# Kernel optimization log

Measured on AMD Instinct MI355X. Metric: run time of the kernel, lower is better.

## Reference

```python
import jax, jax.numpy as jnp
import numpy as np
import math

B, S, D, H = 2, 2048, 1024, 16
DK = D // H


def setup_inputs() -> dict:
    key = jax.random.key(0)
    ks = jax.random.split(key, 12)
    scale = 1.0 / math.sqrt(D)
    inp = {
        "q": jax.random.normal(ks[0], (B, S, D), jnp.float32),
        "k": jax.random.normal(ks[1], (B, S, D), jnp.float32),
        "v": jax.random.normal(ks[2], (B, S, D), jnp.float32),
        # causal mask, broadcast over batch and heads; 0 entries are masked out
        "mask": jnp.tril(jnp.ones((S, S), jnp.int32))[None, None, :, :],
        "wq_w": jax.random.normal(ks[3], (D, D), jnp.float32) * scale,
        "wq_b": jax.random.normal(ks[4], (D,), jnp.float32) * 0.01,
        "wk_w": jax.random.normal(ks[5], (D, D), jnp.float32) * scale,
        "wk_b": jax.random.normal(ks[6], (D,), jnp.float32) * 0.01,
        "wv_w": jax.random.normal(ks[7], (D, D), jnp.float32) * scale,
        "wv_b": jax.random.normal(ks[8], (D,), jnp.float32) * 0.01,
        "wo_w": jax.random.normal(ks[9], (D, D), jnp.float32) * scale,
        "wo_b": jax.random.normal(ks[10], (D,), jnp.float32) * 0.01,
    }
    return inp


def _mha(q, k, v, mask, wq_w, wq_b, wk_w, wk_b, wv_w, wv_b, wo_w, wo_b):
    # nn.Linear: x @ W^T + b
    def split_heads(x):  # [B,S,D] -> [B,H,S,DK]
        return x.reshape(B, S, H, DK).transpose(0, 2, 1, 3)

    Q = split_heads(q @ wq_w.T + wq_b)
    K = split_heads(k @ wk_w.T + wk_b)
    V = split_heads(v @ wv_w.T + wv_b)

    scores = jnp.einsum("bhqd,bhkd->bhqk", Q, K) / math.sqrt(DK)  # [B,H,S,S]
    scores = jnp.where(mask == 0, jnp.float32(-1e9), scores)
    # NOTE: source uses softmax(dim=1) == over the HEADS axis; replicated faithfully.
    attn = jax.nn.softmax(scores, axis=1)
    out = jnp.einsum("bhqk,bhkd->bhqd", attn, V)  # [B,H,S,DK]
    out = out.transpose(0, 2, 1, 3).reshape(B, S, D)
    return out @ wo_w.T + wo_b


def reference(q, k, v, mask, wq_w, wq_b, wk_w, wk_b, wv_w, wv_b, wo_w, wo_b):
    return _mha(q, k, v, mask, wq_w, wq_b, wk_w, wk_b, wv_w, wv_b, wo_w, wo_b)
```

## Files before the change

kernel.cpp:

```cpp
#include <hip/hip_runtime.h>
#include <stdint.h>


#define BB 2
#define SS 2048
#define DD 1024
#define HH 16
#define DKK 64

typedef _Float16 f16;
typedef __attribute__((ext_vector_type(2))) _Float16 f16x2;
typedef __attribute__((ext_vector_type(8))) _Float16 f16x8;
typedef __attribute__((ext_vector_type(2))) __fp16 fp16x2_raw;
typedef __attribute__((ext_vector_type(4))) float f32x4;

typedef __attribute__((address_space(3))) uint32_t lds32_t;
typedef __attribute__((address_space(1))) uint32_t g32_t;

__device__ __forceinline__ void async_cp16(void* lds, const void* g){
    __builtin_amdgcn_global_load_lds((const g32_t*)g, (lds32_t*)lds, 16, 0, 0);
}

union U32H { uint32_t u; f16x2 h; fp16x2_raw hr; };

__device__ __forceinline__ uint32_t pk2(float a, float b){
    U32H c; c.hr = __builtin_amdgcn_cvt_pkrtz(a, b); return c.u;
}
__device__ __forceinline__ float h_lo(uint32_t w){ U32H c; c.u = w; return (float)c.h[0]; }
__device__ __forceinline__ float h_hi(uint32_t w){ U32H c; c.u = w; return (float)c.h[1]; }
__device__ __forceinline__ uint32_t pkmul(uint32_t a, uint32_t b){
    U32H x, y, r; x.u = a; y.u = b; r.h = x.h * y.h; return r.u;
}
__device__ __forceinline__ uint32_t pkadd(uint32_t a, uint32_t b){
    U32H x, y, r; x.u = a; y.u = b; r.h = x.h + y.h; return r.u;
}
__device__ __forceinline__ uint16_t f2h(float f){
    union { f16 h; uint16_t u; } c; c.h = (f16)f; return c.u;
}

__global__ __launch_bounds__(256) void cvt_all(
    const float* __restrict__ w0, const float* __restrict__ w1,
    const float* __restrict__ w2, const float* __restrict__ w3,
    const float* __restrict__ a0, const float* __restrict__ a1,
    const float* __restrict__ a2,
    uint16_t* __restrict__ dw0, uint16_t* __restrict__ dw1,
    uint16_t* __restrict__ dw2, uint16_t* __restrict__ dw3,
    uint16_t* __restrict__ da0, uint16_t* __restrict__ da1,
    uint16_t* __restrict__ da2)
{
    const int id = blockIdx.x;
    const float* s; uint16_t* d; int i;
    if (id < 4096) {
        const int y = id >> 10;
        s = (y==0) ? w0 : (y==1) ? w1 : (y==2) ? w2 : w3;
        d = (y==0) ? dw0 : (y==1) ? dw1 : (y==2) ? dw2 : dw3;
        i = (id & 1023) * 256 + threadIdx.x;
    } else {
        const int id2 = id - 4096;
        const int y = id2 >> 12;
        s = (y==0) ? a0 : (y==1) ? a1 : a2;
        d = (y==0) ? da0 : (y==1) ? da1 : da2;
        i = (id2 & 4095) * 256 + threadIdx.x;
    }
    float4 v = ((const float4*)s)[i];
    ((uint2*)d)[i] = make_uint2(pk2(v.x, v.y), pk2(v.z, v.w));
}

template <int OMODE, int SUMA>
__device__ __forceinline__ void gemm_core(
    uint16_t (*As)[32], uint16_t (*Bs)[32],
    const uint16_t* __restrict__ A, const uint16_t* __restrict__ W,
    const float* __restrict__ bias, void* __restrict__ Cout,
    const int kbeg, const int kend)
{
    const int t    = threadIdx.x;
    const int bm   = blockIdx.x * 128;
    const int bn   = blockIdx.y * 128;
    const int lane = t & 63;
    const int w    = t >> 6;
    const int wm   = (w >> 1) * 64;
    const int wn   = (w & 1) * 64;
    const int lm   = lane & 15;
    const int quad = lane >> 4;

    f32x4 acc[4][4] = {};

    const int lr = lane >> 2;
    const int lc = (lane & 3) * 8;
    const size_t PS = (size_t)BB * SS * DD;

    for (int k0 = kbeg; k0 < kend; k0 += 32) {
#pragma unroll
        for (int i2 = 0; i2 < 2; ++i2) {
            const int i = w * 2 + i2;
            const size_t aoff = (size_t)(bm + 16*i + lr) * DD + k0 + lc;
            if (SUMA) {
                uint4 u0 = *(const uint4*)&A[aoff];
                uint4 u1 = *(const uint4*)&A[aoff + PS];
                uint4 u2 = *(const uint4*)&A[aoff + 2*PS];
                uint4 u3 = *(const uint4*)&A[aoff + 3*PS];
                uint4 sm;
                sm.x = pkadd(pkadd(u0.x, u1.x), pkadd(u2.x, u3.x));
                sm.y = pkadd(pkadd(u0.y, u1.y), pkadd(u2.y, u3.y));
                sm.z = pkadd(pkadd(u0.z, u1.z), pkadd(u2.z, u3.z));
                sm.w = pkadd(pkadd(u0.w, u1.w), pkadd(u2.w, u3.w));
                *(uint4*)&As[16*i + lr][lc] = sm;
            } else {
                async_cp16(&As[16*i][0], &A[aoff]);
            }
            async_cp16(&Bs[16*i][0], &W[(size_t)(bn + 16*i + lr) * DD + k0 + lc]);
        }
        __syncthreads();
        f16x8 a8[4], b8[4];
#pragma unroll
        for (int mt = 0; mt < 4; ++mt) a8[mt] = *(const f16x8*)&As[wm + 16*mt + lm][quad*8];
#pragma unroll
        for (int nt = 0; nt < 4; ++nt) b8[nt] = *(const f16x8*)&Bs[wn + 16*nt + lm][quad*8];
#pragma unroll
        for (int mt = 0; mt < 4; ++mt)
#pragma unroll
            for (int nt = 0; nt < 4; ++nt)
                acc[mt][nt] = __builtin_amdgcn_mfma_f32_16x16x32_f16(a8[mt], b8[nt], acc[mt][nt], 0, 0, 0);
        __syncthreads();
    }

#pragma unroll
    for (int nt = 0; nt < 4; ++nt) {
        const int ng = bn + wn + 16*nt + lm;
        const float bv = bias ? bias[ng] : 0.0f;
#pragma unroll
        for (int mt = 0; mt < 4; ++mt) {
            const int m0 = bm + wm + 16*mt + quad*4;
            if (OMODE == 1) {
                const int bb = m0 >> 11, s0 = m0 & (SS - 1);
                const int hh = ng >> 6,  dk = ng & 63;
                uint2 wv;
                wv.x = pk2(acc[mt][nt][0] + bv, acc[mt][nt][1] + bv);
                wv.y = pk2(acc[mt][nt][2] + bv, acc[mt][nt][3] + bv);
                *(uint2*)&((uint16_t*)Cout)[(((size_t)(bb*HH + hh))*DKK + dk)*SS + s0] = wv;
            } else {
#pragma unroll
                for (int r = 0; r < 4; ++r) {
                    const int m = m0 + r;
                    const float val = acc[mt][nt][r] + bv;
                    if (OMODE == 0) {
                        const int bb = m >> 11, s = m & (SS - 1);
                        const int hh = ng >> 6, dk = ng & 63;
                        ((uint16_t*)Cout)[(((size_t)(bb*HH + hh))*SS + s)*DKK + dk] = f2h(val);
                    } else {
                        ((float*)Cout)[(size_t)m * DD + ng] = val;
                    }
                }
            }
        }
    }
}

__global__ __launch_bounds__(256) void gemm_qkv(
    const uint16_t* __restrict__ xq, const uint16_t* __restrict__ wq,
    const float* __restrict__ bq, uint16_t* __restrict__ Qc,
    const uint16_t* __restrict__ xk, const uint16_t* __restrict__ wk,
    const float* __restrict__ bk, uint16_t* __restrict__ Kc,
    const uint16_t* __restrict__ xv, const uint16_t* __restrict__ wv,
    const float* __restrict__ bv, uint16_t* __restrict__ Vt)
{
    __shared__ __align__(16) uint16_t As[128][32];
    __shared__ __align__(16) uint16_t Bs[128][32];
    const int z = blockIdx.z;
    if (z == 0)      gemm_core<0,0>(As, Bs, xq, wq, bq, Qc, 0, DD);
    else if (z == 1) gemm_core<0,0>(As, Bs, xk, wk, bk, Kc, 0, DD);
    else             gemm_core<1,0>(As, Bs, xv, wv, bv, Vt, 0, DD);
}

__global__ __launch_bounds__(256) void gemm_o_split(
    const uint16_t* __restrict__ A, const uint16_t* __restrict__ W,
    const float* __restrict__ bias, float* __restrict__ P0, float* __restrict__ P1)
{
    __shared__ __align__(16) uint16_t As[128][32];
    __shared__ __align__(16) uint16_t Bs[128][32];
    const int z = blockIdx.z;
    if (z == 0) gemm_core<2,1>(As, Bs, A, W, bias,    (void*)P0, 0,   512);
    else        gemm_core<2,1>(As, Bs, A, W, nullptr, (void*)P1, 512, 1024);
}

__global__ __launch_bounds__(256) void addf4(
    const float* __restrict__ a, const float* __restrict__ b, float* __restrict__ o)
{
    const int i = blockIdx.x * 256 + threadIdx.x;
    float4 x = ((const float4*)a)[i];
    float4 y = ((const float4*)b)[i];
    ((float4*)o)[i] = make_float4(x.x+y.x, x.y+y.y, x.z+y.z, x.w+y.w);
}

__global__ __launch_bounds__(1024) void suf_kernel(
    const uint16_t* __restrict__ Vt, float* __restrict__ Suf)
{
    const int bh = blockIdx.x;
    const int t  = threadIdx.x;
    const int d = t & 63, seg = t >> 6;
    __shared__ float cs[64][65];
    const uint16_t* row = Vt + ((size_t)bh * DKK + d) * SS;
#pragma unroll
    for (int cl = 0; cl < 4; ++cl) {
        const int c = seg * 4 + cl;
        float sum = 0.f;
#pragma unroll
        for (int jj = 0; jj < 4; ++jj) {
            uint4 u = *(const uint4*)&row[c * 32 + jj * 8];
            sum += ((h_lo(u.x)+h_hi(u.x)) + (h_lo(u.y)+h_hi(u.y)))
                 + ((h_lo(u.z)+h_hi(u.z)) + (h_lo(u.w)+h_hi(u.w)));
        }
        cs[c][d] = sum;
    }
    __syncthreads();
    if (t < 64) {
        float run = 0.f;
        Suf[((size_t)bh * 65 + 64) * DKK + t] = 0.f;
        for (int c = 63; c >= 0; --c) {
            run += cs[c][t];
            Suf[((size_t)bh * 65 + c) * DKK + t] = run;
        }
    }
}

__global__ __launch_bounds__(1024) void attn_v9(
    const uint16_t* __restrict__ Qc, const uint16_t* __restrict__ Kc,
    const uint16_t* __restrict__ Vt, const float* __restrict__ Suf,
    uint16_t* __restrict__ AOp)
{
    __shared__ __align__(16) uint16_t E[3][16][32][40];
    __shared__ __align__(16) uint16_t Zr[2][32][40];

    const int x  = blockIdx.x;
    const int p  = x & 3;
    const int b  = (x >> 2) & 1;
    const int pr = x >> 3;
    const int tid  = threadIdx.x;
    const int h    = tid >> 6;
    const int lane = tid & 63;
    const int lm   = lane & 15;
    const int quad = lane >> 4;

    const uint16_t* Qh = Qc + ((size_t)(b*HH + h)) * SS * DKK;
    const uint16_t* Kh = Kc + ((size_t)(b*HH + h)) * SS * DKK;
    const uint16_t* Vh = Vt + ((size_t)(b*HH + h)) * DKK * SS;
    uint16_t* AOb = AOp + ((size_t)(p*BB + b)) * SS * DD;

    const int rq  = tid >> 4;
    const int rk2 = tid & 15;

#pragma unroll
    for (int tt = 0; tt < 2; ++tt) {
        const int tq = tt ? (63 - pr) : pr;
        const int q0 = tq * 32;
        const int nch = (tq >= p) ? ((tq - p) >> 2) + 1 : 0;

        f16x8 qf[2][2];
#pragma unroll
        for (int qt = 0; qt < 2; ++qt)
#pragma unroll
            for (int kd = 0; kd < 2; ++kd)
                qf[qt][kd] = *(const f16x8*)&Qh[(size_t)(q0 + 16*qt + lm)*DKK + kd*32 + quad*8];

        f32x4 oacc[2][4] = {};

        auto SCORES = [&](int c, int ebw) {
            const int k0 = c * 32;
            f32x4 sacc[2][2] = {};
#pragma unroll
            for (int kt = 0; kt < 2; ++kt) {
                f16x8 kf0 = *(const f16x8*)&Kh[(size_t)(k0 + 16*kt + lm)*DKK + quad*8];
                f16x8 kf1 = *(const f16x8*)&Kh[(size_t)(k0 + 16*kt + lm)*DKK + 32 + quad*8];
#pragma unroll
                for (int qt = 0; qt < 2; ++qt) {
                    sacc[kt][qt] = __builtin_amdgcn_mfma_f32_16x16x32_f16(kf0, qf[qt][0], sacc[kt][qt], 0, 0, 0);
                    sacc[kt][qt] = __builtin_amdgcn_mfma_f32_16x16x32_f16(kf1, qf[qt][1], sacc[kt][qt], 0, 0, 0);
                }
            }
#pragma unroll
            for (int kt = 0; kt < 2; ++kt)
#pragma unroll
                for (int qt = 0; qt < 2; ++qt) {
                    const int qg = q0 + 16*qt + lm;
                    float e[4];
#pragma unroll
                    for (int r = 0; r < 4; ++r) {
                        const int kg = k0 + 16*kt + quad*4 + r;
                        e[r] = (kg > qg) ? 1.0f : __expf(sacc[kt][qt][r] * 0.125f);
                    }
                    *(uint2*)&E[ebw][h][16*qt + lm][16*kt + quad*4] =
                        make_uint2(pk2(e[0], e[1]), pk2(e[2], e[3]));
                }
        };

        auto HEADSUM = [&](int ebr, int zbw) {
            float z0 = 0.f, z1 = 0.f;
#pragma unroll
            for (int i = 0; i < 16; ++i) {
                uint32_t wv2 = *(const uint32_t*)&E[ebr][i][rq][rk2*2];
                z0 += h_lo(wv2); z1 += h_hi(wv2);
            }
            *(uint32_t*)&Zr[zbw][rq][rk2*2] = pk2(__fdividef(1.f, z0), __fdividef(1.f, z1));
        };

        auto PV = [&](int c, int ebr, int zbr) {
            const int k0 = c * 32;
            f16x8 vf[4];
#pragma unroll
            for (int dt = 0; dt < 4; ++dt)
                vf[dt] = *(const f16x8*)&Vh[(size_t)(16*dt + lm)*SS + k0 + quad*8];
#pragma unroll
            for (int qt = 0; qt < 2; ++qt) {
                uint4 eu = *(const uint4*)&E[ebr][h][16*qt + lm][quad*8];
                uint4 zu = *(const uint4*)&Zr[zbr][16*qt + lm][quad*8];
                union { uint4 u; f16x8 v; } P;
                P.u.x = pkmul(eu.x, zu.x); P.u.y = pkmul(eu.y, zu.y);
                P.u.z = pkmul(eu.z, zu.z); P.u.w = pkmul(eu.w, zu.w);
#pragma unroll
                for (int dt = 0; dt < 4; ++dt)
                    oacc[qt][dt] = __builtin_amdgcn_mfma_f32_16x16x32_f16(P.v, vf[dt], oacc[qt][dt], 0, 0, 0);
            }
        };

        __syncthreads();

        if (nch > 0) {
            SCORES(p, 0);
            __syncthreads();
            int eb = 0;
            for (int n = 0; n < nch; ++n) {
                const int c  = p + 4*n;
                const int zb = n & 1;
                if (tid < 512) HEADSUM(eb, zb);
                if (n > 0)       PV(c - 4, (eb + 2) % 3, zb ^ 1);
                if (n + 1 < nch) SCORES(c + 4, (eb + 1) % 3);
                __syncthreads();
                eb = (eb + 1 == 3) ? 0 : eb + 1;
            }
            PV(p + 4*(nch - 1), (eb + 2) % 3, (nch - 1) & 1);
        }

        float corr[4] = {0.f, 0.f, 0.f, 0.f};
        if (p == 0) {
            const float* Sf = Suf + ((size_t)(b*HH + h) * 65 + (tq + 1)) * DKK;
#pragma unroll
            for (int dt = 0; dt < 4; ++dt) corr[dt] = 0.0625f * Sf[16*dt + lm];
        }
#pragma unroll
        for (int qt = 0; qt < 2; ++qt)
#pragma unroll
            for (int dt = 0; dt < 4; ++dt)
#pragma unroll
                for (int r = 0; r < 4; ++r) {
                    const int s = q0 + 16*qt + quad*4 + r;
                    AOb[(size_t)s * DD + h*DKK + 16*dt + lm] = f2h(oacc[qt][dt][r] + corr[dt]);
                }
    }
}

extern "C" void kernel_launch(void* const* d_in, const int* in_sizes, int n_in,
                              void* d_out, int out_size, void* d_ws, size_t ws_size,
                              hipStream_t stream)
{
    const float* q    = (const float*)d_in[0];
    const float* k    = (const float*)d_in[1];
    const float* v    = (const float*)d_in[2];
    const float* wq_w = (const float*)d_in[4];
    const float* wq_b = (const float*)d_in[5];
    const float* wk_w = (const float*)d_in[6];
    const float* wk_b = (const float*)d_in[7];
    const float* wv_w = (const float*)d_in[8];
    const float* wv_b = (const float*)d_in[9];
    const float* wo_w = (const float*)d_in[10];
    const float* wo_b = (const float*)d_in[11];
    float* out = (float*)d_out;

    uint16_t* wsu = (uint16_t*)d_ws;
    const size_t M1 = (size_t)1 << 20;
    uint16_t* wcq = wsu + 0 * M1;
    uint16_t* wck = wsu + 1 * M1;
    uint16_t* wcv = wsu + 2 * M1;
    uint16_t* wco = wsu + 3 * M1;
    uint16_t* Qc  = wsu + 4 * M1;
    uint16_t* Kc  = wsu + 8 * M1;
    uint16_t* Vt  = wsu + 12 * M1;
    uint16_t* AOp = wsu + 16 * M1;
    uint16_t* xq  = wsu + 16 * M1;
    uint16_t* xk  = wsu + 20 * M1;
    uint16_t* xv  = wsu + 24 * M1;
    float*    Suf = (float*)wcq;
    float*    P1  = (float*)(wsu + 4 * M1);

    cvt_all<<<16384, 256, 0, stream>>>(
        wq_w, wk_w, wv_w, wo_w, q, k, v,
        wcq, wck, wcv, wco, xq, xk, xv);

    gemm_qkv<<<dim3(32, 8, 3), 256, 0, stream>>>(
        xq, wcq, wq_b, Qc,
        xk, wck, wk_b, Kc,
        xv, wcv, wv_b, Vt);

    suf_kernel<<<32, 1024, 0, stream>>>(Vt, Suf);
    attn_v9<<<256, 1024, 0, stream>>>(Qc, Kc, Vt, Suf, AOp);

    gemm_o_split<<<dim3(32, 8, 2), 256, 0, stream>>>(AOp, wco, wo_b, out, P1);
    addf4<<<4096, 256, 0, stream>>>(out, P1, out);
}
```

Measured before the change: 291.2 us.

## Split attention into one query tile per block, drop software pipelining

The attention kernel now launches 512 blocks, each handling a single 32-row query tile, where before 256 blocks each processed a paired light and heavy tile. The triple-buffered E and double-buffered Zr pipeline (scores of the next chunk overlapped with headsum and PV of the current one) is replaced by a plain sequential loop with three barriers per chunk. This cuts LDS use and aims for better occupancy and load balance across the larger grid. In exchange it gives up overlap between phases and adds synchronisation stalls, and the per-block work becomes more uneven because causal tiles differ in length.

```diff
diff --git a/kernel.cpp b/kernel.cpp
--- a/kernel.cpp
+++ b/kernel.cpp
@@ -223,18 +223,19 @@
     }
 }
 
-__global__ __launch_bounds__(1024) void attn_v9(
+__global__ __launch_bounds__(1024) void attn_v15(
     const uint16_t* __restrict__ Qc, const uint16_t* __restrict__ Kc,
     const uint16_t* __restrict__ Vt, const float* __restrict__ Suf,
     uint16_t* __restrict__ AOp)
 {
-    __shared__ __align__(16) uint16_t E[3][16][32][40];
-    __shared__ __align__(16) uint16_t Zr[2][32][40];
+    __shared__ __align__(16) uint16_t E[16][32][40];
+    __shared__ __align__(16) uint16_t Zr[32][40];
 
     const int x  = blockIdx.x;
     const int p  = x & 3;
     const int b  = (x >> 2) & 1;
-    const int pr = x >> 3;
+    const int j  = x >> 3;
+    const int tq = (j < 32) ? j : 95 - j;
     const int tid  = threadIdx.x;
     const int h    = tid >> 6;
     const int lane = tid & 63;
@@ -249,70 +250,65 @@
     const int rq  = tid >> 4;
     const int rk2 = tid & 15;
 
-#pragma unroll
-    for (int tt = 0; tt < 2; ++tt) {
-        const int tq = tt ? (63 - pr) : pr;
-        const int q0 = tq * 32;
-        const int nch = (tq >= p) ? ((tq - p) >> 2) + 1 : 0;
-
-        f16x8 qf[2][2];
-#pragma unroll
-        for (int qt = 0; qt < 2; ++qt)
-#pragma unroll
-            for (int kd = 0; kd < 2; ++kd)
-                qf[qt][kd] = *(const f16x8*)&Qh[(size_t)(q0 + 16*qt + lm)*DKK + kd*32 + quad*8];
-
-        f32x4 oacc[2][4] = {};
-
-        auto SCORES = [&](int c, int ebw) {
-            const int k0 = c * 32;
-            f32x4 sacc[2][2] = {};
-#pragma unroll
-            for (int kt = 0; kt < 2; ++kt) {
-                f16x8 kf0 = *(const f16x8*)&Kh[(size_t)(k0 + 16*kt + lm)*DKK + quad*8];
-                f16x8 kf1 = *(const f16x8*)&Kh[(size_t)(k0 + 16*kt + lm)*DKK + 32 + quad*8];
-#pragma unroll
-                for (int qt = 0; qt < 2; ++qt) {
-                    sacc[kt][qt] = __builtin_amdgcn_mfma_f32_16x16x32_f16(kf0, qf[qt][0], sacc[kt][qt], 0, 0, 0);
-                    sacc[kt][qt] = __builtin_amdgcn_mfma_f32_16x16x32_f16(kf1, qf[qt][1], sacc[kt][qt], 0, 0, 0);
+    const int q0 = tq * 32;
+
+    f16x8 qf[2][2];
+#pragma unroll
+    for (int qt = 0; qt < 2; ++qt)
+#pragma unroll
+        for (int kd = 0; kd < 2; ++kd)
+            qf[qt][kd] = *(const f16x8*)&Qh[(size_t)(q0 + 16*qt + lm)*DKK + kd*32 + quad*8];
+
+    f32x4 oacc[2][4] = {};
+
+    for (int c = p; c <= tq; c += 4) {
+        const int k0 = c * 32;
+        f32x4 sacc[2][2] = {};
+#pragma unroll
+        for (int kt = 0; kt < 2; ++kt) {
+            f16x8 kf0 = *(const f16x8*)&Kh[(size_t)(k0 + 16*kt + lm)*DKK + quad*8];
+            f16x8 kf1 = *(const f16x8*)&Kh[(size_t)(k0 + 16*kt + lm)*DKK + 32 + quad*8];
+#pragma unroll
+            for (int qt = 0; qt < 2; ++qt) {
+                sacc[kt][qt] = __builtin_amdgcn_mfma_f32_16x16x32_f16(kf0, qf[qt][0], sacc[kt][qt], 0, 0, 0);
+                sacc[kt][qt] = __builtin_amdgcn_mfma_f32_16x16x32_f16(kf1, qf[qt][1], sacc[kt][qt], 0, 0, 0);
+            }
+        }
+        __syncthreads();
+#pragma unroll
+        for (int kt = 0; kt < 2; ++kt)
+#pragma unroll
+            for (int qt = 0; qt < 2; ++qt) {
+                const int qg = q0 + 16*qt + lm;
+                float e[4];
+#pragma unroll
+                for (int r = 0; r < 4; ++r) {
+                    const int kg = k0 + 16*kt + quad*4 + r;
+                    e[r] = (kg > qg) ? 1.0f : __expf(sacc[kt][qt][r] * 0.125f);
                 }
-            }
-#pragma unroll
-            for (int kt = 0; kt < 2; ++kt)
-#pragma unroll
-                for (int qt = 0; qt < 2; ++qt) {
-                    const int qg = q0 + 16*qt + lm;
-                    float e[4];
-#pragma unroll
-                    for (int r = 0; r < 4; ++r) {
-                        const int kg = k0 + 16*kt + quad*4 + r;
-                        e[r] = (kg > qg) ? 1.0f : __expf(sacc[kt][qt][r] * 0.125f);
-                    }
-                    *(uint2*)&E[ebw][h][16*qt + lm][16*kt + quad*4] =
-                        make_uint2(pk2(e[0], e[1]), pk2(e[2], e[3]));
-                }
-        };
-
-        auto HEADSUM = [&](int ebr, int zbw) {
+                *(uint2*)&E[h][16*qt + lm][16*kt + quad*4] =
+                    make_uint2(pk2(e[0], e[1]), pk2(e[2], e[3]));
+            }
+        __syncthreads();
+        if (tid < 512) {
             float z0 = 0.f, z1 = 0.f;
 #pragma unroll
             for (int i = 0; i < 16; ++i) {
-                uint32_t wv2 = *(const uint32_t*)&E[ebr][i][rq][rk2*2];
+                uint32_t wv2 = *(const uint32_t*)&E[i][rq][rk2*2];
                 z0 += h_lo(wv2); z1 += h_hi(wv2);
             }
-            *(uint32_t*)&Zr[zbw][rq][rk2*2] = pk2(__fdividef(1.f, z0), __fdividef(1.f, z1));
-        };
-
-        auto PV = [&](int c, int ebr, int zbr) {
-            const int k0 = c * 32;
+            *(uint32_t*)&Zr[rq][rk2*2] = pk2(__fdividef(1.f, z0), __fdividef(1.f, z1));
+        }
+        __syncthreads();
+        {
             f16x8 vf[4];
 #pragma unroll
             for (int dt = 0; dt < 4; ++dt)
                 vf[dt] = *(const f16x8*)&Vh[(size_t)(16*dt + lm)*SS + k0 + quad*8];
 #pragma unroll
             for (int qt = 0; qt < 2; ++qt) {
-                uint4 eu = *(const uint4*)&E[ebr][h][16*qt + lm][quad*8];
-                uint4 zu = *(const uint4*)&Zr[zbr][16*qt + lm][quad*8];
+                uint4 eu = *(const uint4*)&E[h][16*qt + lm][quad*8];
+                uint4 zu = *(const uint4*)&Zr[16*qt + lm][quad*8];
                 union { uint4 u; f16x8 v; } P;
                 P.u.x = pkmul(eu.x, zu.x); P.u.y = pkmul(eu.y, zu.y);
                 P.u.z = pkmul(eu.z, zu.z); P.u.w = pkmul(eu.w, zu.w);
@@ -320,42 +316,24 @@
                 for (int dt = 0; dt < 4; ++dt)
                     oacc[qt][dt] = __builtin_amdgcn_mfma_f32_16x16x32_f16(P.v, vf[dt], oacc[qt][dt], 0, 0, 0);
             }
-        };
-
-        __syncthreads();
-
-        if (nch > 0) {
-            SCORES(p, 0);
-            __syncthreads();
-            int eb = 0;
-            for (int n = 0; n < nch; ++n) {
-                const int c  = p + 4*n;
-                const int zb = n & 1;
-                if (tid < 512) HEADSUM(eb, zb);
-                if (n > 0)       PV(c - 4, (eb + 2) % 3, zb ^ 1);
-                if (n + 1 < nch) SCORES(c + 4, (eb + 1) % 3);
-                __syncthreads();
-                eb = (eb + 1 == 3) ? 0 : eb + 1;
-            }
-            PV(p + 4*(nch - 1), (eb + 2) % 3, (nch - 1) & 1);
-        }
-
-        float corr[4] = {0.f, 0.f, 0.f, 0.f};
-        if (p == 0) {
-            const float* Sf = Suf + ((size_t)(b*HH + h) * 65 + (tq + 1)) * DKK;
-#pragma unroll
-            for (int dt = 0; dt < 4; ++dt) corr[dt] = 0.0625f * Sf[16*dt + lm];
-        }
-#pragma unroll
-        for (int qt = 0; qt < 2; ++qt)
-#pragma unroll
-            for (int dt = 0; dt < 4; ++dt)
-#pragma unroll
-                for (int r = 0; r < 4; ++r) {
-                    const int s = q0 + 16*qt + quad*4 + r;
-                    AOb[(size_t)s * DD + h*DKK + 16*dt + lm] = f2h(oacc[qt][dt][r] + corr[dt]);
-                }
-    }
+        }
+    }
+
+    float corr[4] = {0.f, 0.f, 0.f, 0.f};
+    if (p == 0) {
+        const float* Sf = Suf + ((size_t)(b*HH + h) * 65 + (tq + 1)) * DKK;
+#pragma unroll
+        for (int dt = 0; dt < 4; ++dt) corr[dt] = 0.0625f * Sf[16*dt + lm];
+    }
+#pragma unroll
+    for (int qt = 0; qt < 2; ++qt)
+#pragma unroll
+        for (int dt = 0; dt < 4; ++dt)
+#pragma unroll
+            for (int r = 0; r < 4; ++r) {
+                const int s = q0 + 16*qt + quad*4 + r;
+                AOb[(size_t)s * DD + h*DKK + 16*dt + lm] = f2h(oacc[qt][dt][r] + corr[dt]);
+            }
 }
 
 extern "C" void kernel_launch(void* const* d_in, const int* in_sizes, int n_in,
@@ -401,7 +379,7 @@
         xv, wcv, wv_b, Vt);
 
     suf_kernel<<<32, 1024, 0, stream>>>(Vt, Suf);
-    attn_v9<<<256, 1024, 0, stream>>>(Qc, Kc, Vt, Suf, AOp);
+    attn_v15<<<512, 1024, 0, stream>>>(Qc, Kc, Vt, Suf, AOp);
 
     gemm_o_split<<<dim3(32, 8, 2), 256, 0, stream>>>(AOp, wco, wo_b, out, P1);
     addf4<<<4096, 256, 0, stream>>>(out, P1, out);
```

Result: slower. 299.7 us (+3.0%).
